# Performance work log

Hardware: AMD Instinct MI355X
Metric: run time of the kernel (lower is better)

Reference implementation:

```python
import jax, jax.numpy as jnp
import numpy as np

N, M, F = 4096, 8192, 512  # central nodes, unique neighbors, feature dim
ALPHA = 0.2                # LeakyReLU negative slope
NEG = -9e15                # masked-out attention logit (matches torch code)


def setup_inputs() -> dict:
    key = jax.random.key(0)
    k1, k2, k3, k4, k5 = jax.random.split(key, 5)
    node_feats = jax.random.normal(k1, (N, F), jnp.float32)
    neighbor_feats = jax.random.normal(k2, (M, F), jnp.float32)
    # xavier-style scaled init for the learned params
    weight = jax.random.normal(k3, (F, F), jnp.float32) * (1.0 / np.sqrt(F))
    att_weight = jax.random.normal(k4, (2 * F, 1), jnp.float32) * (1.0 / np.sqrt(2 * F))
    # binary adjacency mask: mask[i, j] = 1 if unique-neighbor j is a neighbor of node i
    mask = jax.random.randint(k5, (N, M), 0, 2, jnp.int32)
    return {"node_feats": node_feats, "neighbor_feats": neighbor_feats,
            "weight": weight, "att_weight": att_weight, "mask": mask}


def reference(node_feats, neighbor_feats, weight, att_weight, mask):
    # GAT-mode aggregation. The torch code materializes a_input [N, M, 2F] and
    # multiplies by att_weight; since a^T [h_i || h_j] = a1^T h_i + a2^T h_j,
    # we compute the identical scores without the N*M*2F intermediate.
    Wh_n = node_feats @ weight        # [N, F]
    Wh_m = neighbor_feats @ weight    # [M, F]
    f = weight.shape[1]
    a1 = att_weight[:f, 0]            # [F]
    a2 = att_weight[f:, 0]            # [F]
    scores = (Wh_n @ a1)[:, None] + (Wh_m @ a2)[None, :]   # [N, M]
    scores = jnp.where(scores > 0, scores, ALPHA * scores)  # LeakyReLU(0.2)
    scores = jnp.where(mask > 0, scores, NEG)
    attention = jax.nn.softmax(scores, axis=1)               # [N, M]
    return attention @ Wh_m                                  # [N, F]
```

## Files before the change

kernel.cpp:

```cpp
#include <hip/hip_runtime.h>
#include <stdint.h>

#define LOG2E 1.44269504088896340736f

using bf16x8 = __attribute__((ext_vector_type(8))) short;
using f32x4  = __attribute__((ext_vector_type(4))) float;

__device__ __forceinline__ ushort f2bf(float f) {
  union { float f; uint32_t u; } v; v.f = f;
  uint32_t u = v.u;
  u += 0x7FFFu + ((u >> 16) & 1u);
  return (ushort)(u >> 16);
}
__device__ __forceinline__ float bf2f(ushort b) {
  union { uint32_t u; float f; } v; v.u = ((uint32_t)b) << 16;
  return v.f;
}

__device__ __forceinline__ void load_lds16(const void* g, void* l) {
  __builtin_amdgcn_global_load_lds(
      (const __attribute__((address_space(1))) void*)g,
      (__attribute__((address_space(3))) void*)l, 16, 0, 0);
}

__global__ void rowdot(const float* __restrict__ mat, const float* __restrict__ vec,
                       float* __restrict__ out) {
  int w = threadIdx.x >> 6, l = threadIdx.x & 63;
  int row = blockIdx.x * 4 + w;
  const float4* mp = (const float4*)(mat + row * 512 + l * 8);
  const float4* vp = (const float4*)(vec + l * 8);
  float4 a0 = mp[0], a1 = mp[1];
  float4 b0 = vp[0], b1 = vp[1];
  float d = a0.x * b0.x + a0.y * b0.y + a0.z * b0.z + a0.w * b0.w
          + a1.x * b1.x + a1.y * b1.y + a1.z * b1.z + a1.w * b1.w;
#pragma unroll
  for (int o = 32; o > 0; o >>= 1) d += __shfl_xor(d, o, 64);
  if (l == 0) out[row] = d;
}

__global__ void reduce_max(const float* __restrict__ v, float* __restrict__ outmax) {
  __shared__ float red[4];
  int t = threadIdx.x;
  float m = -3.0e38f;
  for (int j = t; j < 8192; j += 256) m = fmaxf(m, v[j]);
#pragma unroll
  for (int o = 32; o > 0; o >>= 1) m = fmaxf(m, __shfl_xor(m, o, 64));
  if ((t & 63) == 0) red[t >> 6] = m;
  __syncthreads();
  if (t == 0) outmax[0] = fmaxf(fmaxf(red[0], red[1]), fmaxf(red[2], red[3]));
}

__global__ void cvt4_bf16(const float* __restrict__ in, ushort* __restrict__ out) {
  int idx = blockIdx.x * 256 + threadIdx.x;
  float4 v = ((const float4*)in)[idx];
  ushort4 o; o.x = f2bf(v.x); o.y = f2bf(v.y); o.z = f2bf(v.z); o.w = f2bf(v.w);
  ((ushort4*)out)[idx] = o;
}

__global__ void transpose_w(const float* __restrict__ w, ushort* __restrict__ wT) {
  __shared__ float tile[32][33];
  int t = threadIdx.x; int tx = t & 31, ty = t >> 5;
  int cb = (blockIdx.x & 15) * 32, fb = (blockIdx.x >> 4) * 32;
#pragma unroll
  for (int k = 0; k < 4; ++k) tile[ty + k * 8][tx] = w[(cb + ty + k * 8) * 512 + fb + tx];
  __syncthreads();
#pragma unroll
  for (int k = 0; k < 4; ++k) wT[(fb + ty + k * 8) * 512 + cb + tx] = f2bf(tile[tx][ty + k * 8]);
}

__global__ __launch_bounds__(256, 4) void gemm_whmT(const ushort* __restrict__ A,
                                                    const ushort* __restrict__ B,
                                                    ushort* __restrict__ WhmT) {
  __shared__ ushort At[128 * 32];
  __shared__ ushort Bt2[128 * 32];
  int t = threadIdx.x;
  int j0 = (blockIdx.x >> 2) * 128, f0 = (blockIdx.x & 3) * 128;
  int w = t >> 6, l = t & 63, wr = w >> 1, wc = w & 1;
  f32x4 acc[4][4] = {};
  for (int it = 0; it < 16; ++it) {
    int k0 = it * 32;
#pragma unroll
    for (int c = 0; c < 2; ++c) {
      int u = c * 256 + t; int rr = u >> 2, p = u & 3;
      int sg = p ^ ((rr >> 1) & 3);
      load_lds16(A + (j0 + rr) * 512 + k0 + sg * 8, At + (c * 256 + (t & ~63)) * 8);
      load_lds16(B + (f0 + rr) * 512 + k0 + sg * 8, Bt2 + (c * 256 + (t & ~63)) * 8);
    }
    __syncthreads();
    bf16x8 af[4], bfr[4];
#pragma unroll
    for (int m = 0; m < 4; ++m) {
      int rr = wr * 64 + m * 16 + (l & 15);
      int q = (l >> 4) ^ ((rr >> 1) & 3);
      af[m] = *(const bf16x8*)(At + rr * 32 + q * 8);
    }
#pragma unroll
    for (int n = 0; n < 4; ++n) {
      int rb = wc * 64 + n * 16 + (l & 15);
      int q = (l >> 4) ^ ((rb >> 1) & 3);
      bfr[n] = *(const bf16x8*)(Bt2 + rb * 32 + q * 8);
    }
#pragma unroll
    for (int m = 0; m < 4; ++m)
#pragma unroll
      for (int n = 0; n < 4; ++n)
        acc[m][n] = __builtin_amdgcn_mfma_f32_16x16x32_bf16(af[m], bfr[n], acc[m][n], 0, 0, 0);
    __syncthreads();
  }
#pragma unroll
  for (int m = 0; m < 4; ++m)
#pragma unroll
    for (int n = 0; n < 4; ++n) {
      int j = j0 + wr * 64 + m * 16 + (l >> 4) * 4;
      int f = f0 + wc * 64 + n * 16 + (l & 15);
      ushort4 o;
      o.x = f2bf(acc[m][n][0]); o.y = f2bf(acc[m][n][1]);
      o.z = f2bf(acc[m][n][2]); o.w = f2bf(acc[m][n][3]);
      *(ushort4*)(WhmT + f * 8192 + j) = o;
    }
}

__global__ __launch_bounds__(512, 4) void attn_main(
    const ushort* __restrict__ WhmT, const int* __restrict__ mask,
    const float* __restrict__ s_n, const float* __restrict__ s_m,
    const float* __restrict__ smaxp, ushort* __restrict__ num, float* __restrict__ den) {
  __shared__ ushort Bt[2][512 * 32];
  __shared__ ushort Pt[2][64 * 32];
  int t = threadIdx.x;
  int bid = blockIdx.x;
  int s = bid & 7;
  int rblk = bid >> 3;
  int i0 = rblk * 64;
  int kb = s * 1024;
  int w = t >> 6, l = t & 63, l15 = l & 15;
  int i_loc = t >> 3, jt = t & 7;

  float sn = s_n[i0 + i_loc];
  float smx = smaxp[0];
  float mz = sn + smx;
  float m_i = mz > 0.f ? mz : 0.2f * mz;
  float miL = m_i * LOG2E;
  float dacc = 0.f;
  f32x4 acc[4][4] = {};

  int psP = (jt >> 1) ^ ((i_loc >> 1) & 3);
  ushort* pw0 = &Pt[0][0] + i_loc * 32 + psP * 8 + (jt & 1) * 4;
  ushort* pw1 = &Pt[1][0] + i_loc * 32 + psP * 8 + (jt & 1) * 4;
  int qA = (l >> 4) ^ ((l15 >> 1) & 3);
  const ushort* pa0 = &Pt[0][0] + l15 * 32 + qA * 8;
  const ushort* pa1 = &Pt[1][0] + l15 * 32 + qA * 8;
  const ushort* pb0 = &Bt[0][0] + (w * 64 + l15) * 32 + qA * 8;
  const ushort* pb1 = &Bt[1][0] + (w * 64 + l15) * 32 + qA * 8;

  const int* mrow = mask + (size_t)(i0 + i_loc) * 8192 + kb + jt * 4;
  const float* sptr = s_m + kb + jt * 4;

#define STAGE_B(BUF_, T_)                                                     \
  {                                                                           \
    int k0_ = kb + (T_) * 32;                                                 \
    ushort* bb_ = BUF_;                                                       \
    _Pragma("unroll") for (int c = 0; c < 4; ++c) {                           \
      int u_ = c * 512 + t; int rr_ = u_ >> 2, p_ = u_ & 3;                   \
      int sg_ = p_ ^ ((rr_ >> 1) & 3);                                        \
      load_lds16(WhmT + rr_ * 8192 + k0_ + sg_ * 8,                           \
                 bb_ + (c * 512 + (t & ~63)) * 8);                            \
    }                                                                         \
  }

#define P_COMP(mkv, svv, pdst)                                                \
  {                                                                           \
    float z0 = sn + (svv).x, z1 = sn + (svv).y;                               \
    float z2 = sn + (svv).z, z3 = sn + (svv).w;                               \
    float e0 = (z0 > 0.f ? z0 : 0.2f * z0) * LOG2E - miL;                     \
    float e1 = (z1 > 0.f ? z1 : 0.2f * z1) * LOG2E - miL;                     \
    float e2 = (z2 > 0.f ? z2 : 0.2f * z2) * LOG2E - miL;                     \
    float e3 = (z3 > 0.f ? z3 : 0.2f * z3) * LOG2E - miL;                     \
    float p0 = (mkv).x > 0 ? exp2f(e0) : 0.f;                                 \
    float p1 = (mkv).y > 0 ? exp2f(e1) : 0.f;                                 \
    float p2 = (mkv).z > 0 ? exp2f(e2) : 0.f;                                 \
    float p3 = (mkv).w > 0 ? exp2f(e3) : 0.f;                                 \
    ushort4 pv;                                                               \
    pv.x = f2bf(p0); pv.y = f2bf(p1); pv.z = f2bf(p2); pv.w = f2bf(p3);       \
    dacc += bf2f(pv.x) + bf2f(pv.y) + bf2f(pv.z) + bf2f(pv.w);                \
    *(ushort4*)(pdst) = pv;                                                   \
  }

#define BODY(IT_, PA_, PB_, PW_, DO_P, DO_STAGE)                              \
  {                                                                           \
    if (DO_STAGE) { STAGE_B((((IT_) & 1) ? &Bt[0][0] : &Bt[1][0]), (IT_) + 1); } \
    if (DO_P) { P_COMP(mkR, svR, PW_); }                                      \
    if (DO_STAGE) {                                                           \
      int kM_ = (((IT_) + 2) & 31) * 32;                                      \
      mkR = *(const int4*)(mrow + kM_);                                       \
      svR = *(const float4*)(sptr + kM_);                                     \
    }                                                                         \
    __builtin_amdgcn_sched_barrier(0);                                        \
    asm volatile("s_waitcnt lgkmcnt(0)\n\ts_barrier" ::: "memory");           \
    __builtin_amdgcn_sched_barrier(0);                                        \
    bf16x8 af[4];                                                             \
    _Pragma("unroll") for (int m = 0; m < 4; ++m)                             \
      af[m] = *(const bf16x8*)(PA_ + m * 512);                                \
    __builtin_amdgcn_s_setprio(1);                                            \
    _Pragma("unroll") for (int n = 0; n < 4; ++n) {                           \
      bf16x8 bfr = *(const bf16x8*)(PB_ + n * 512);                           \
      _Pragma("unroll") for (int m = 0; m < 4; ++m)                           \
        acc[m][n] = __builtin_amdgcn_mfma_f32_16x16x32_bf16(af[m], bfr,       \
                                                            acc[m][n], 0, 0, 0); \
    }                                                                         \
    __builtin_amdgcn_s_setprio(0);                                            \
    asm volatile("s_barrier" ::: "memory");                                   \
  }

  STAGE_B(&Bt[0][0], 0);
  int4 mkR; float4 svR;
  {
    int4 mk0 = *(const int4*)(mrow);
    float4 sv0 = *(const float4*)(sptr);
    P_COMP(mk0, sv0, pw0);
  }
  mkR = *(const int4*)(mrow + 32);
  svR = *(const float4*)(sptr + 32);
  __builtin_amdgcn_sched_barrier(0);
  asm volatile("s_waitcnt lgkmcnt(0)\n\ts_barrier" ::: "memory");
  __builtin_amdgcn_sched_barrier(0);

  for (int it2 = 0; it2 < 15; ++it2) {
    int it = it2 * 2;
    BODY(it,     pa0, pb0, pw1, true, true);
    BODY(it + 1, pa1, pb1, pw0, true, true);
  }
  BODY(30, pa0, pb0, pw1, true, true);
  BODY(31, pa1, pb1, pw0, false, false);

  dacc += __shfl_xor(dacc, 4, 64);
  dacc += __shfl_xor(dacc, 2, 64);
  dacc += __shfl_xor(dacc, 1, 64);
  if ((t & 7) == 0) den[s * 4096 + i0 + i_loc] = dacc;
#pragma unroll
  for (int m = 0; m < 4; ++m)
#pragma unroll
    for (int n = 0; n < 4; ++n) {
      int ig = rblk * 16 + m * 4 + (l >> 4);
      int f = w * 64 + n * 16 + l15;
      ushort4 o;
      o.x = f2bf(acc[m][n][0]); o.y = f2bf(acc[m][n][1]);
      o.z = f2bf(acc[m][n][2]); o.w = f2bf(acc[m][n][3]);
      *(ushort4*)(num + (((size_t)s * 1024 + ig) * 512 + f) * 4) = o;
    }
#undef BODY
#undef P_COMP
#undef STAGE_B
}

__global__ void reduce_out(const ushort* __restrict__ num, const float* __restrict__ den,
                           float* __restrict__ out) {
  int idx = blockIdx.x * 256 + threadIdx.x;
  int ig = idx >> 9, f = idx & 511;
  float s0 = 0.f, s1 = 0.f, s2 = 0.f, s3 = 0.f;
#pragma unroll
  for (int s = 0; s < 8; ++s) {
    ushort4 v = *(const ushort4*)(num + (((size_t)s * 1024 + ig) * 512 + f) * 4);
    s0 += bf2f(v.x); s1 += bf2f(v.y); s2 += bf2f(v.z); s3 += bf2f(v.w);
  }
  float d0 = 0.f, d1 = 0.f, d2 = 0.f, d3 = 0.f;
#pragma unroll
  for (int s = 0; s < 8; ++s) {
    const float* dp = den + s * 4096 + ig * 4;
    d0 += dp[0]; d1 += dp[1]; d2 += dp[2]; d3 += dp[3];
  }
  float* op = out + (size_t)ig * 4 * 512 + f;
  op[0]        = s0 / d0;
  op[512]      = s1 / d1;
  op[2 * 512]  = s2 / d2;
  op[3 * 512]  = s3 / d3;
}

extern "C" void kernel_launch(void* const* d_in, const int* in_sizes, int n_in,
                              void* d_out, int out_size, void* d_ws, size_t ws_size,
                              hipStream_t stream) {
  const float* node   = (const float*)d_in[0];
  const float* neigh  = (const float*)d_in[1];
  const float* weight = (const float*)d_in[2];
  const float* att    = (const float*)d_in[3];
  const int*   mask   = (const int*)d_in[4];
  float* out = (float*)d_out;

  char* ws = (char*)d_ws;
  float* w_a1 = (float*)ws;
  float* w_a2 = w_a1 + 512;
  float* s_n  = w_a2 + 512;
  float* s_m  = s_n + 4096;
  float* smax = s_m + 8192;
  ushort* neigh_bf = (ushort*)(ws + 64 * 1024);
  ushort* wT_bf    = neigh_bf + 8192 * 512;
  ushort* WhmT     = wT_bf + 512 * 512;
  ushort* num      = WhmT + 512 * 8192;
  float*  den      = (float*)(num + (size_t)8 * 1024 * 512 * 4);

  rowdot<<<128, 256, 0, stream>>>(weight, att, w_a1);
  rowdot<<<128, 256, 0, stream>>>(weight, att + 512, w_a2);
  rowdot<<<1024, 256, 0, stream>>>(node, w_a1, s_n);
  rowdot<<<2048, 256, 0, stream>>>(neigh, w_a2, s_m);
  reduce_max<<<1, 256, 0, stream>>>(s_m, smax);
  cvt4_bf16<<<4096, 256, 0, stream>>>(neigh, neigh_bf);
  transpose_w<<<256, 256, 0, stream>>>(weight, wT_bf);
  gemm_whmT<<<256, 256, 0, stream>>>(neigh_bf, wT_bf, WhmT);
  attn_main<<<512, 512, 0, stream>>>(WhmT, mask, s_n, s_m, smax, num, den);
  reduce_out<<<2048, 256, 0, stream>>>(num, den, out);
}
```

Baseline: 112.8 us.

## Factor softmax exponent into separable terms and split P into separate pass

Rewrites exp(leakyrelu(sn+sm)-m) as the max of two products of precomputed per-row and per-column exponentials, removing per-element exp calls. The probability matrix is now written to global memory in bf16 by a standalone kernel, with its denominator computed there. A separate GEMM kernel then streams P through LDS. This trades in-kernel exp work for an extra 64MB write and re-read of P, and it adds kernel launches. The factored products can overflow or underflow in ways the original exponent did not.

```diff
diff --git a/kernel.cpp b/kernel.cpp
--- a/kernel.cpp
+++ b/kernel.cpp
@@ -21,6 +21,11 @@
   __builtin_amdgcn_global_load_lds(
       (const __attribute__((address_space(1))) void*)g,
       (__attribute__((address_space(3))) void*)l, 16, 0, 0);
+}
+__device__ __forceinline__ void load_lds4(const void* g, void* l) {
+  __builtin_amdgcn_global_load_lds(
+      (const __attribute__((address_space(1))) void*)g,
+      (__attribute__((address_space(3))) void*)l, 4, 0, 0);
 }
 
 __global__ void rowdot(const float* __restrict__ mat, const float* __restrict__ vec,
@@ -48,6 +53,24 @@
   if ((t & 63) == 0) red[t >> 6] = m;
   __syncthreads();
   if (t == 0) outmax[0] = fmaxf(fmaxf(red[0], red[1]), fmaxf(red[2], red[3]));
+}
+
+__global__ void exp_sm(const float* __restrict__ s_m, float* __restrict__ E1,
+                       float* __restrict__ E2) {
+  int j = blockIdx.x * 256 + threadIdx.x;
+  float v = s_m[j];
+  E1[j] = exp2f(v * LOG2E);
+  E2[j] = exp2f(v * (0.2f * LOG2E));
+}
+
+__global__ void comp_A(const float* __restrict__ s_n, const float* __restrict__ smaxp,
+                       float* __restrict__ A1, float* __restrict__ A2) {
+  int i = blockIdx.x * 256 + threadIdx.x;
+  float sn = s_n[i];
+  float mz = sn + smaxp[0];
+  float mi = fmaxf(mz, 0.2f * mz);
+  A1[i] = exp2f((sn - mi) * LOG2E);
+  A2[i] = exp2f((0.2f * sn - mi) * LOG2E);
 }
 
 __global__ void cvt4_bf16(const float* __restrict__ in, ushort* __restrict__ out) {
@@ -120,40 +143,75 @@
     }
 }
 
-__global__ __launch_bounds__(512, 4) void attn_main(
-    const ushort* __restrict__ WhmT, const int* __restrict__ mask,
-    const float* __restrict__ s_n, const float* __restrict__ s_m,
-    const float* __restrict__ smaxp, ushort* __restrict__ num, float* __restrict__ den) {
+__global__ __launch_bounds__(256) void p_mat(
+    const int* __restrict__ mask, const float* __restrict__ A1f,
+    const float* __restrict__ A2f, const float* __restrict__ E1,
+    const float* __restrict__ E2, ushort* __restrict__ P,
+    float* __restrict__ den_part) {
+  int row = blockIdx.x, t = threadIdx.x;
+  float a1 = A1f[row], a2 = A2f[row];
+  const int* mrow = mask + (size_t)row * 8192;
+  ushort* prow = P + (size_t)row * 8192;
+#pragma unroll
+  for (int iter = 0; iter < 4; ++iter) {
+    int j8 = (iter * 256 + t) * 8;
+    int4 k0 = *(const int4*)(mrow + j8);
+    int4 k1 = *(const int4*)(mrow + j8 + 4);
+    float4 e1a = *(const float4*)(E1 + j8), e1b = *(const float4*)(E1 + j8 + 4);
+    float4 e2a = *(const float4*)(E2 + j8), e2b = *(const float4*)(E2 + j8 + 4);
+    float p0 = k0.x ? fmaxf(a1 * e1a.x, a2 * e2a.x) : 0.f;
+    float p1 = k0.y ? fmaxf(a1 * e1a.y, a2 * e2a.y) : 0.f;
+    float p2 = k0.z ? fmaxf(a1 * e1a.z, a2 * e2a.z) : 0.f;
+    float p3 = k0.w ? fmaxf(a1 * e1a.w, a2 * e2a.w) : 0.f;
+    float p4 = k1.x ? fmaxf(a1 * e1b.x, a2 * e2b.x) : 0.f;
+    float p5 = k1.y ? fmaxf(a1 * e1b.y, a2 * e2b.y) : 0.f;
+    float p6 = k1.z ? fmaxf(a1 * e1b.z, a2 * e2b.z) : 0.f;
+    float p7 = k1.w ? fmaxf(a1 * e1b.w, a2 * e2b.w) : 0.f;
+    ushort b0 = f2bf(p0), b1 = f2bf(p1), b2 = f2bf(p2), b3 = f2bf(p3);
+    ushort b4 = f2bf(p4), b5 = f2bf(p5), b6 = f2bf(p6), b7 = f2bf(p7);
+    uint4 pk;
+    pk.x = ((uint32_t)b1 << 16) | b0;
+    pk.y = ((uint32_t)b3 << 16) | b2;
+    pk.z = ((uint32_t)b5 << 16) | b4;
+    pk.w = ((uint32_t)b7 << 16) | b6;
+    *(uint4*)(prow + j8) = pk;
+    float d = ((bf2f(b0) + bf2f(b1)) + (bf2f(b2) + bf2f(b3)))
+            + ((bf2f(b4) + bf2f(b5)) + (bf2f(b6) + bf2f(b7)));
+#pragma unroll
+    for (int o = 32; o > 0; o >>= 1) d += __shfl_xor(d, o, 64);
+    if ((t & 63) == 0) den_part[row * 16 + iter * 4 + (t >> 6)] = d;
+  }
+}
+
+__global__ void p_den(const float* __restrict__ den_part, float* __restrict__ den) {
+  int i = blockIdx.x * 256 + threadIdx.x;
+  const float* dp = den_part + i * 16;
+  float d = 0.f;
+#pragma unroll
+  for (int k = 0; k < 16; ++k) d += dp[k];
+  den[i] = d;
+}
+
+__global__ __launch_bounds__(512, 4) void attn_gemm(
+    const ushort* __restrict__ P, const ushort* __restrict__ WhmT,
+    ushort* __restrict__ num) {
   __shared__ ushort Bt[2][512 * 32];
-  __shared__ ushort Pt[2][64 * 32];
+  __shared__ ushort At[2][64 * 32];
   int t = threadIdx.x;
   int bid = blockIdx.x;
   int s = bid & 7;
   int rblk = bid >> 3;
   int i0 = rblk * 64;
   int kb = s * 1024;
-  int w = t >> 6, l = t & 63, l15 = l & 15;
-  int i_loc = t >> 3, jt = t & 7;
-
-  float sn = s_n[i0 + i_loc];
-  float smx = smaxp[0];
-  float mz = sn + smx;
-  float m_i = mz > 0.f ? mz : 0.2f * mz;
-  float miL = m_i * LOG2E;
-  float dacc = 0.f;
+  int w = t >> 6, l = t & 63, l15 = l & 15, lq = l >> 4;
+
   f32x4 acc[4][4] = {};
 
-  int psP = (jt >> 1) ^ ((i_loc >> 1) & 3);
-  ushort* pw0 = &Pt[0][0] + i_loc * 32 + psP * 8 + (jt & 1) * 4;
-  ushort* pw1 = &Pt[1][0] + i_loc * 32 + psP * 8 + (jt & 1) * 4;
-  int qA = (l >> 4) ^ ((l15 >> 1) & 3);
-  const ushort* pa0 = &Pt[0][0] + l15 * 32 + qA * 8;
-  const ushort* pa1 = &Pt[1][0] + l15 * 32 + qA * 8;
+  int qA = lq ^ ((l15 >> 1) & 3);
+  const ushort* pa0 = &At[0][0] + l15 * 32 + qA * 8;
+  const ushort* pa1 = &At[1][0] + l15 * 32 + qA * 8;
   const ushort* pb0 = &Bt[0][0] + (w * 64 + l15) * 32 + qA * 8;
   const ushort* pb1 = &Bt[1][0] + (w * 64 + l15) * 32 + qA * 8;
-
-  const int* mrow = mask + (size_t)(i0 + i_loc) * 8192 + kb + jt * 4;
-  const float* sptr = s_m + kb + jt * 4;
 
 #define STAGE_B(BUF_, T_)                                                     \
   {                                                                           \
@@ -166,37 +224,23 @@
                  bb_ + (c * 512 + (t & ~63)) * 8);                            \
     }                                                                         \
   }
-
-#define P_COMP(mkv, svv, pdst)                                                \
+#define STAGE_A(BUF_, T_)                                                     \
   {                                                                           \
-    float z0 = sn + (svv).x, z1 = sn + (svv).y;                               \
-    float z2 = sn + (svv).z, z3 = sn + (svv).w;                               \
-    float e0 = (z0 > 0.f ? z0 : 0.2f * z0) * LOG2E - miL;                     \
-    float e1 = (z1 > 0.f ? z1 : 0.2f * z1) * LOG2E - miL;                     \
-    float e2 = (z2 > 0.f ? z2 : 0.2f * z2) * LOG2E - miL;                     \
-    float e3 = (z3 > 0.f ? z3 : 0.2f * z3) * LOG2E - miL;                     \
-    float p0 = (mkv).x > 0 ? exp2f(e0) : 0.f;                                 \
-    float p1 = (mkv).y > 0 ? exp2f(e1) : 0.f;                                 \
-    float p2 = (mkv).z > 0 ? exp2f(e2) : 0.f;                                 \
-    float p3 = (mkv).w > 0 ? exp2f(e3) : 0.f;                                 \
-    ushort4 pv;                                                               \
-    pv.x = f2bf(p0); pv.y = f2bf(p1); pv.z = f2bf(p2); pv.w = f2bf(p3);       \
-    dacc += bf2f(pv.x) + bf2f(pv.y) + bf2f(pv.z) + bf2f(pv.w);                \
-    *(ushort4*)(pdst) = pv;                                                   \
-  }
-
-#define BODY(IT_, PA_, PB_, PW_, DO_P, DO_STAGE)                              \
+    int k0_ = kb + (T_) * 32;                                                 \
+    ushort* ab_ = BUF_;                                                       \
+    _Pragma("unroll") for (int c = 0; c < 2; ++c) {                           \
+      int u_ = c * 512 + t; int row_ = u_ >> 4, g_ = u_ & 15;                 \
+      int col_ = (((g_ >> 2) ^ ((row_ >> 1) & 3)) << 3) + (g_ & 3) * 2;       \
+      load_lds4(P + (size_t)(i0 + row_) * 8192 + k0_ + col_,                  \
+                ab_ + (c * 512 + (t & ~63)) * 2);                             \
+    }                                                                         \
+  }
+
+#define BODY(IT_, PA_, PB_, BN_, AN_, DO_STAGE, VMC_)                         \
   {                                                                           \
-    if (DO_STAGE) { STAGE_B((((IT_) & 1) ? &Bt[0][0] : &Bt[1][0]), (IT_) + 1); } \
-    if (DO_P) { P_COMP(mkR, svR, PW_); }                                      \
-    if (DO_STAGE) {                                                           \
-      int kM_ = (((IT_) + 2) & 31) * 32;                                      \
-      mkR = *(const int4*)(mrow + kM_);                                       \
-      svR = *(const float4*)(sptr + kM_);                                     \
-    }                                                                         \
-    __builtin_amdgcn_sched_barrier(0);                                        \
-    asm volatile("s_waitcnt lgkmcnt(0)\n\ts_barrier" ::: "memory");           \
-    __builtin_amdgcn_sched_barrier(0);                                        \
+    if (DO_STAGE) { STAGE_B(BN_, (IT_) + 1); STAGE_A(AN_, (IT_) + 1); }       \
+    asm volatile("s_waitcnt vmcnt(" #VMC_ ")" ::: "memory");                  \
+    __builtin_amdgcn_s_barrier();                                             \
     bf16x8 af[4];                                                             \
     _Pragma("unroll") for (int m = 0; m < 4; ++m)                             \
       af[m] = *(const bf16x8*)(PA_ + m * 512);                                \
@@ -212,35 +256,22 @@
   }
 
   STAGE_B(&Bt[0][0], 0);
-  int4 mkR; float4 svR;
-  {
-    int4 mk0 = *(const int4*)(mrow);
-    float4 sv0 = *(const float4*)(sptr);
-    P_COMP(mk0, sv0, pw0);
-  }
-  mkR = *(const int4*)(mrow + 32);
-  svR = *(const float4*)(sptr + 32);
-  __builtin_amdgcn_sched_barrier(0);
-  asm volatile("s_waitcnt lgkmcnt(0)\n\ts_barrier" ::: "memory");
-  __builtin_amdgcn_sched_barrier(0);
+  STAGE_A(&At[0][0], 0);
+  asm volatile("s_waitcnt vmcnt(0)" ::: "memory");
+  __builtin_amdgcn_s_barrier();
 
   for (int it2 = 0; it2 < 15; ++it2) {
-    int it = it2 * 2;
-    BODY(it,     pa0, pb0, pw1, true, true);
-    BODY(it + 1, pa1, pb1, pw0, true, true);
-  }
-  BODY(30, pa0, pb0, pw1, true, true);
-  BODY(31, pa1, pb1, pw0, false, false);
-
-  dacc += __shfl_xor(dacc, 4, 64);
-  dacc += __shfl_xor(dacc, 2, 64);
-  dacc += __shfl_xor(dacc, 1, 64);
-  if ((t & 7) == 0) den[s * 4096 + i0 + i_loc] = dacc;
+    BODY(it2 * 2,     pa0, pb0, &Bt[1][0], &At[1][0], true, 6);
+    BODY(it2 * 2 + 1, pa1, pb1, &Bt[0][0], &At[0][0], true, 6);
+  }
+  BODY(30, pa0, pb0, &Bt[1][0], &At[1][0], true, 6);
+  BODY(31, pa1, pb1, &Bt[0][0], &At[0][0], false, 0);
+
 #pragma unroll
   for (int m = 0; m < 4; ++m)
 #pragma unroll
     for (int n = 0; n < 4; ++n) {
-      int ig = rblk * 16 + m * 4 + (l >> 4);
+      int ig = rblk * 16 + m * 4 + lq;
       int f = w * 64 + n * 16 + l15;
       ushort4 o;
       o.x = f2bf(acc[m][n][0]); o.y = f2bf(acc[m][n][1]);
@@ -248,7 +279,7 @@
       *(ushort4*)(num + (((size_t)s * 1024 + ig) * 512 + f) * 4) = o;
     }
 #undef BODY
-#undef P_COMP
+#undef STAGE_A
 #undef STAGE_B
 }
 
@@ -262,17 +293,12 @@
     ushort4 v = *(const ushort4*)(num + (((size_t)s * 1024 + ig) * 512 + f) * 4);
     s0 += bf2f(v.x); s1 += bf2f(v.y); s2 += bf2f(v.z); s3 += bf2f(v.w);
   }
-  float d0 = 0.f, d1 = 0.f, d2 = 0.f, d3 = 0.f;
-#pragma unroll
-  for (int s = 0; s < 8; ++s) {
-    const float* dp = den + s * 4096 + ig * 4;
-    d0 += dp[0]; d1 += dp[1]; d2 += dp[2]; d3 += dp[3];
-  }
+  const float* dp = den + ig * 4;
   float* op = out + (size_t)ig * 4 * 512 + f;
-  op[0]        = s0 / d0;
-  op[512]      = s1 / d1;
-  op[2 * 512]  = s2 / d2;
-  op[3 * 512]  = s3 / d3;
+  op[0]       = s0 / dp[0];
+  op[512]     = s1 / dp[1];
+  op[2 * 512] = s2 / dp[2];
+  op[3 * 512] = s3 / dp[3];
 }
 
 extern "C" void kernel_launch(void* const* d_in, const int* in_sizes, int n_in,
@@ -286,25 +312,36 @@
   float* out = (float*)d_out;
 
   char* ws = (char*)d_ws;
-  float* w_a1 = (float*)ws;
-  float* w_a2 = w_a1 + 512;
-  float* s_n  = w_a2 + 512;
-  float* s_m  = s_n + 4096;
-  float* smax = s_m + 8192;
-  ushort* neigh_bf = (ushort*)(ws + 64 * 1024);
-  ushort* wT_bf    = neigh_bf + 8192 * 512;
-  ushort* WhmT     = wT_bf + 512 * 512;
-  ushort* num      = WhmT + 512 * 8192;
-  float*  den      = (float*)(num + (size_t)8 * 1024 * 512 * 4);
+  float* fb = (float*)ws;
+  float* w_a1    = fb;
+  float* w_a2    = fb + 512;
+  float* s_n     = fb + 1024;
+  float* s_m     = fb + 5120;
+  float* smax    = fb + 13312;
+  float* A1      = fb + 13320;
+  float* A2      = fb + 17416;
+  float* E1      = fb + 21512;
+  float* E2      = fb + 29704;
+  float* den_part= fb + 37896;
+  float* den     = fb + 103432;
+  ushort* wT_bf  = (ushort*)(ws + 512 * 1024);
+  ushort* WhmT   = (ushort*)(ws + 1 * 1024 * 1024);
+  ushort* num    = (ushort*)(ws + 9 * 1024 * 1024);
+  ushort* P      = (ushort*)(ws + 41 * 1024 * 1024);
+  ushort* neigh_bf = P;
 
   rowdot<<<128, 256, 0, stream>>>(weight, att, w_a1);
   rowdot<<<128, 256, 0, stream>>>(weight, att + 512, w_a2);
   rowdot<<<1024, 256, 0, stream>>>(node, w_a1, s_n);
   rowdot<<<2048, 256, 0, stream>>>(neigh, w_a2, s_m);
   reduce_max<<<1, 256, 0, stream>>>(s_m, smax);
+  exp_sm<<<32, 256, 0, stream>>>(s_m, E1, E2);
+  comp_A<<<16, 256, 0, stream>>>(s_n, smax, A1, A2);
   cvt4_bf16<<<4096, 256, 0, stream>>>(neigh, neigh_bf);
   transpose_w<<<256, 256, 0, stream>>>(weight, wT_bf);
   gemm_whmT<<<256, 256, 0, stream>>>(neigh_bf, wT_bf, WhmT);
-  attn_main<<<512, 512, 0, stream>>>(WhmT, mask, s_n, s_m, smax, num, den);
+  p_mat<<<4096, 256, 0, stream>>>(mask, A1, A2, E1, E2, P, den_part);
+  p_den<<<16, 256, 0, stream>>>(den_part, den);
+  attn_gemm<<<512, 512, 0, stream>>>(P, WhmT, num);
   reduce_out<<<2048, 256, 0, stream>>>(num, den, out);
 }
```

Result: slower. 162.5 us (+44.0%).
